# Kernel tuning notes

Measured on AMD Instinct MI355X. Metric: run time of the kernel, lower is better.

Reference implementation:

```python
import jax, jax.numpy as jnp
import numpy as np
from jax import lax

SEQ_LEN = 256
BAT = 128
TAGSET = 64
START_TAG = 62
END_TAG = 63
AVERAGE_BATCH = True


def setup_inputs() -> dict:
    key = jax.random.key(0)
    k1, k2 = jax.random.split(key)
    scores = jax.random.normal(k1, (SEQ_LEN, BAT, TAGSET, TAGSET), dtype=jnp.float32)
    target = jax.random.randint(k2, (SEQ_LEN, BAT, 1), 0, TAGSET * TAGSET, dtype=jnp.int64)
    mask = jnp.ones((SEQ_LEN, BAT), dtype=bool)
    corpus_mask = jnp.ones((1, BAT, 1, TAGSET), dtype=jnp.float32)
    return {"scores": scores, "corpus_mask": corpus_mask, "target": target, "mask": mask}


def _crf_loss(scores, target, mask):
    seq_len, bat, T, _ = scores.shape
    # gold path energy: gather flattened (prev_tag, cur_tag) scores at target indices
    flat = scores.reshape(seq_len, bat, T * T)
    tg = jnp.take_along_axis(flat, target, axis=2)[..., 0]  # [seq_len, bat]
    tg_energy = jnp.sum(jnp.where(mask, tg, 0.0))

    # forward algorithm (log partition) as a scan over time
    init = scores[0, :, START_TAG, :]  # [bat, T]

    def step(carry, inp):
        cur_partition, partition = carry
        cur_values, m = inp  # [bat, T, T], [bat]
        cv = cur_values + cur_partition[:, :, None]          # add prev-tag partition
        new_cur = jax.nn.logsumexp(cv, axis=1)               # [bat, T]
        # switch: where mask is on, take updated partition; else keep old
        new_part = jnp.where(m[:, None], new_cur, partition)
        return (new_cur, new_part), None

    (_, partition), _ = lax.scan(step, (init, init), (scores[1:], mask[1:]))
    log_Z = jnp.sum(partition[:, END_TAG])

    loss = log_Z - tg_energy
    if AVERAGE_BATCH:
        loss = loss / bat
    return loss


def reference(scores, corpus_mask, target, mask):
    # corpus_mask is unused in the unrestricted forward path (as in the original module)
    return _crf_loss(scores, target, mask)
```

## Files before the change

### kernel.cpp

```cpp
#include <hip/hip_runtime.h>

#define NBAT 128
#define NT 64
#define SEQ 256
#define START_TAG 62
#define END_TAG 63

__global__ void zero_out_kernel(float* out) { out[0] = 0.0f; }

__global__ __launch_bounds__(64) void crf_loss_kernel(
    const float* __restrict__ scores,
    const int* __restrict__ target,
    float* __restrict__ out)
{
    const int b    = blockIdx.x;
    const int lane = threadIdx.x;
    const int g    = lane >> 4;
    const int c    = lane & 15;

    __shared__ float cur[NT];

    const size_t matsz   = (size_t)NT * NT;
    const size_t bstride = (size_t)NBAT * matsz;

    float tg = 0.0f;
    for (int t = lane; t < SEQ; t += 64) {
        int idx = target[t * NBAT + b];
        tg += scores[(size_t)t * bstride + (size_t)b * matsz + (size_t)idx];
    }
    #pragma unroll
    for (int off = 1; off < 64; off <<= 1) tg += __shfl_xor(tg, off);

    const float* m0 = scores + (size_t)b * matsz;
    float4 ic = *(const float4*)(m0 + START_TAG * NT + c * 4);
    if (g == 0) *(float4*)(&cur[c * 4]) = ic;
    float C = fmaxf(fmaxf(ic.x, ic.y), fmaxf(ic.z, ic.w));
    #pragma unroll
    for (int off = 1; off < 16; off <<= 1) C = fmaxf(C, __shfl_xor(C, off));

    const int laneoff = g * NT + c * 4;

    float4 v[16], nv[16];
    float4 nc = make_float4(0.f, 0.f, 0.f, 0.f);

    auto step = [&](const float4* vv) {
        float4 s4 = make_float4(0.f, 0.f, 0.f, 0.f);
        #pragma unroll
        for (int r = 0; r < 16; ++r) {
            float cc = cur[g + 4 * r] - C;
            s4.x += __expf(vv[r].x + cc);
            s4.y += __expf(vv[r].y + cc);
            s4.z += __expf(vv[r].z + cc);
            s4.w += __expf(vv[r].w + cc);
        }
        s4.x += __shfl_xor(s4.x, 16); s4.y += __shfl_xor(s4.y, 16);
        s4.z += __shfl_xor(s4.z, 16); s4.w += __shfl_xor(s4.w, 16);
        s4.x += __shfl_xor(s4.x, 32); s4.y += __shfl_xor(s4.y, 32);
        s4.z += __shfl_xor(s4.z, 32); s4.w += __shfl_xor(s4.w, 32);
        nc.x = C + __logf(s4.x);
        nc.y = C + __logf(s4.y);
        nc.z = C + __logf(s4.z);
        nc.w = C + __logf(s4.w);
        if (g == 0) *(float4*)(&cur[c * 4]) = nc;
        float m = fmaxf(fmaxf(nc.x, nc.y), fmaxf(nc.z, nc.w));
        #pragma unroll
        for (int off = 1; off < 16; off <<= 1) m = fmaxf(m, __shfl_xor(m, off));
        C = m;
    };

    {
        const float* p = scores + bstride + (size_t)b * matsz + laneoff;
        #pragma unroll
        for (int r = 0; r < 16; ++r)
            v[r] = *(const float4*)(p + r * 256);
    }

    for (int t = 1; t < SEQ - 1; t += 2) {
        const float* pn = scores + (size_t)(t + 1) * bstride + (size_t)b * matsz + laneoff;
        #pragma unroll
        for (int r = 0; r < 16; ++r)
            nv[r] = *(const float4*)(pn + r * 256);
        step(v);
        const float* pn2 = scores + (size_t)(t + 2) * bstride + (size_t)b * matsz + laneoff;
        #pragma unroll
        for (int r = 0; r < 16; ++r)
            v[r] = *(const float4*)(pn2 + r * 256);
        step(nv);
    }
    step(v);

    float logZb = __shfl(nc.w, 15);
    if (lane == 0) {
        atomicAdd(out, (logZb - tg) * (1.0f / (float)NBAT));
    }
}

extern "C" void kernel_launch(void* const* d_in, const int* in_sizes, int n_in,
                              void* d_out, int out_size, void* d_ws, size_t ws_size,
                              hipStream_t stream) {
    const float* scores = (const float*)d_in[0];
    const int*   target = (const int*)d_in[2];
    float* out = (float*)d_out;

    hipLaunchKernelGGL(zero_out_kernel, dim3(1), dim3(1), 0, stream, out);
    hipLaunchKernelGGL(crf_loss_kernel, dim3(NBAT), dim3(64), 0, stream,
                       scores, target, out);
}
```

Baseline: 817.2 us.

## Parallelize CRF forward over time chunks via bf16 MFMA matrix products in exp space

Replaces the sequential per-batch log-sum-exp scan with a chunked scheme. Each of 16 time chunks per batch item computes a product of exp-space 64x64 transition matrices using bf16 MFMA, with power-of-two rescaling tracked as integer exponents. A second kernel chains the chunk matrices as vector-matrix products and adds the gold-path energy. This exposes 16x more blocks and puts the work on matrix cores, but bf16 exp-space products lose precision. The exponent tracking guards against overflow, but small entries may underflow.

Result: faster. 751.4 us (-8.0%).

```diff
diff --git a/kernel.cpp b/kernel.cpp
--- a/kernel.cpp
+++ b/kernel.cpp
@@ -1,97 +1,212 @@
 #include <hip/hip_runtime.h>
-
+#include <hip/hip_bf16.h>
+
+#define SEQ 256
 #define NBAT 128
 #define NT 64
-#define SEQ 256
 #define START_TAG 62
 #define END_TAG 63
-
-__global__ void zero_out_kernel(float* out) { out[0] = 0.0f; }
-
-__global__ __launch_bounds__(64) void crf_loss_kernel(
+#define CHUNK 16
+#define NCHUNK (SEQ / CHUNK)
+#define TROW 68
+#define LN2 0.6931471805599453f
+
+typedef __bf16 bf16x8 __attribute__((ext_vector_type(8)));
+typedef float f32x4 __attribute__((ext_vector_type(4)));
+
+__global__ __launch_bounds__(64) void crf_chunk_kernel(
+    const float* __restrict__ scores,
+    __hip_bfloat16* __restrict__ wsT,
+    int* __restrict__ wsK,
+    float* __restrict__ out)
+{
+    const int b    = blockIdx.x & (NBAT - 1);
+    const int c    = blockIdx.x >> 7;
+    const int lane = threadIdx.x;
+    const int quad = lane >> 4;
+    const int l15  = lane & 15;
+
+    if (blockIdx.x == 0 && lane == 0) out[0] = 0.0f;
+
+    __shared__ float Pbuf[NT * NT];
+    __shared__ float Tbuf[NT * TROW];
+
+    const int t0 = c * CHUNK;
+    const size_t matfl = (size_t)NT * NT;
+
+    {
+        const float* m1 = scores + ((size_t)((t0 + 1) * NBAT + b)) * matfl;
+        #pragma unroll
+        for (int q = 0; q < 16; ++q) {
+            __builtin_amdgcn_global_load_lds(
+                (const __attribute__((address_space(1))) unsigned int*)(m1 + q * 256 + lane * 4),
+                (__attribute__((address_space(3))) unsigned int*)(&Pbuf[q * 256]),
+                16, 0, 0);
+        }
+    }
+
+    {
+        const float* m0 = scores + ((size_t)(t0 * NBAT + b)) * matfl;
+        #pragma unroll
+        for (int q = 0; q < 16; ++q) {
+            float4 vv = *(const float4*)(m0 + q * 256 + lane * 4);
+            int f = q * 256 + lane * 4;
+            int row = f >> 6, col = f & 63;
+            float4 e;
+            e.x = __expf(vv.x); e.y = __expf(vv.y);
+            e.z = __expf(vv.z); e.w = __expf(vv.w);
+            *(float4*)(&Tbuf[row * TROW + col]) = e;
+        }
+    }
+
+    float r = 1.0f;
+    int ksum = 0;
+    f32x4 acc[4][4];
+
+    for (int s = 1; s < CHUNK; ++s) {
+        asm volatile("s_waitcnt vmcnt(0)" ::: "memory");
+
+        bf16x8 bf[2][4];
+        #pragma unroll
+        for (int ks = 0; ks < 2; ++ks)
+            #pragma unroll
+            for (int nb = 0; nb < 4; ++nb) {
+                const int n  = nb * 16 + l15;
+                const int k0 = ks * 32 + quad * 8;
+                #pragma unroll
+                for (int j = 0; j < 8; ++j)
+                    bf[ks][nb][j] = (__bf16)__expf(Pbuf[(k0 + j) * 64 + n]);
+            }
+
+        asm volatile("s_waitcnt lgkmcnt(0)" ::: "memory");
+        if (s + 1 < CHUNK) {
+            const float* mn = scores + ((size_t)((t0 + s + 1) * NBAT + b)) * matfl;
+            #pragma unroll
+            for (int q = 0; q < 16; ++q) {
+                __builtin_amdgcn_global_load_lds(
+                    (const __attribute__((address_space(1))) unsigned int*)(mn + q * 256 + lane * 4),
+                    (__attribute__((address_space(3))) unsigned int*)(&Pbuf[q * 256]),
+                    16, 0, 0);
+            }
+        }
+
+        bf16x8 af[4][2];
+        #pragma unroll
+        for (int mb = 0; mb < 4; ++mb)
+            #pragma unroll
+            for (int ks = 0; ks < 2; ++ks) {
+                const int m  = mb * 16 + l15;
+                const int k0 = ks * 32 + quad * 8;
+                float4 lo = *(const float4*)(&Tbuf[m * TROW + k0]);
+                float4 hi = *(const float4*)(&Tbuf[m * TROW + k0 + 4]);
+                af[mb][ks][0] = (__bf16)(lo.x * r);
+                af[mb][ks][1] = (__bf16)(lo.y * r);
+                af[mb][ks][2] = (__bf16)(lo.z * r);
+                af[mb][ks][3] = (__bf16)(lo.w * r);
+                af[mb][ks][4] = (__bf16)(hi.x * r);
+                af[mb][ks][5] = (__bf16)(hi.y * r);
+                af[mb][ks][6] = (__bf16)(hi.z * r);
+                af[mb][ks][7] = (__bf16)(hi.w * r);
+            }
+
+        #pragma unroll
+        for (int mb = 0; mb < 4; ++mb)
+            #pragma unroll
+            for (int nb = 0; nb < 4; ++nb) {
+                f32x4 a0 = {0.f, 0.f, 0.f, 0.f};
+                a0 = __builtin_amdgcn_mfma_f32_16x16x32_bf16(af[mb][0], bf[0][nb], a0, 0, 0, 0);
+                a0 = __builtin_amdgcn_mfma_f32_16x16x32_bf16(af[mb][1], bf[1][nb], a0, 0, 0, 0);
+                acc[mb][nb] = a0;
+            }
+
+        if (s < CHUNK - 1) {
+            float mx = 0.0f;
+            #pragma unroll
+            for (int mb = 0; mb < 4; ++mb)
+                #pragma unroll
+                for (int nb = 0; nb < 4; ++nb)
+                    #pragma unroll
+                    for (int reg = 0; reg < 4; ++reg)
+                        mx = fmaxf(mx, acc[mb][nb][reg]);
+            #pragma unroll
+            for (int off = 1; off < 64; off <<= 1)
+                mx = fmaxf(mx, __shfl_xor(mx, off));
+            const int k = (int)((__float_as_uint(mx) >> 23) & 255u) - 127;
+            ksum += k;
+            r = __uint_as_float((unsigned)(127 - k) << 23);
+
+            #pragma unroll
+            for (int mb = 0; mb < 4; ++mb)
+                #pragma unroll
+                for (int nb = 0; nb < 4; ++nb)
+                    #pragma unroll
+                    for (int reg = 0; reg < 4; ++reg) {
+                        const int row = mb * 16 + quad * 4 + reg;
+                        const int col = nb * 16 + l15;
+                        Tbuf[row * TROW + col] = acc[mb][nb][reg];
+                    }
+        }
+    }
+
+    __hip_bfloat16* Tw = wsT + ((size_t)(b * NCHUNK + c)) * matfl;
+    #pragma unroll
+    for (int mb = 0; mb < 4; ++mb)
+        #pragma unroll
+        for (int nb = 0; nb < 4; ++nb)
+            #pragma unroll
+            for (int reg = 0; reg < 4; ++reg) {
+                const int row = mb * 16 + quad * 4 + reg;
+                const int col = nb * 16 + l15;
+                Tw[row * 64 + col] = __float2bfloat16(acc[mb][nb][reg]);
+            }
+    if (lane == 0) wsK[b * NCHUNK + c] = ksum;
+}
+
+__global__ __launch_bounds__(64) void crf_combine_kernel(
     const float* __restrict__ scores,
     const int* __restrict__ target,
+    const __hip_bfloat16* __restrict__ wsT,
+    const int* __restrict__ wsK,
     float* __restrict__ out)
 {
-    const int b    = blockIdx.x;
+    const int b = blockIdx.x;
     const int lane = threadIdx.x;
-    const int g    = lane >> 4;
-    const int c    = lane & 15;
-
-    __shared__ float cur[NT];
-
-    const size_t matsz   = (size_t)NT * NT;
-    const size_t bstride = (size_t)NBAT * matsz;
 
     float tg = 0.0f;
-    for (int t = lane; t < SEQ; t += 64) {
+    #pragma unroll
+    for (int t4 = 0; t4 < 4; ++t4) {
+        int t = t4 * 64 + lane;
         int idx = target[t * NBAT + b];
-        tg += scores[(size_t)t * bstride + (size_t)b * matsz + (size_t)idx];
+        tg += scores[((size_t)(t * NBAT + b)) * 4096 + (size_t)idx];
     }
     #pragma unroll
     for (int off = 1; off < 64; off <<= 1) tg += __shfl_xor(tg, off);
 
-    const float* m0 = scores + (size_t)b * matsz;
-    float4 ic = *(const float4*)(m0 + START_TAG * NT + c * 4);
-    if (g == 0) *(float4*)(&cur[c * 4]) = ic;
-    float C = fmaxf(fmaxf(ic.x, ic.y), fmaxf(ic.z, ic.w));
-    #pragma unroll
-    for (int off = 1; off < 16; off <<= 1) C = fmaxf(C, __shfl_xor(C, off));
-
-    const int laneoff = g * NT + c * 4;
-
-    float4 v[16], nv[16];
-    float4 nc = make_float4(0.f, 0.f, 0.f, 0.f);
-
-    auto step = [&](const float4* vv) {
-        float4 s4 = make_float4(0.f, 0.f, 0.f, 0.f);
-        #pragma unroll
-        for (int r = 0; r < 16; ++r) {
-            float cc = cur[g + 4 * r] - C;
-            s4.x += __expf(vv[r].x + cc);
-            s4.y += __expf(vv[r].y + cc);
-            s4.z += __expf(vv[r].z + cc);
-            s4.w += __expf(vv[r].w + cc);
-        }
-        s4.x += __shfl_xor(s4.x, 16); s4.y += __shfl_xor(s4.y, 16);
-        s4.z += __shfl_xor(s4.z, 16); s4.w += __shfl_xor(s4.w, 16);
-        s4.x += __shfl_xor(s4.x, 32); s4.y += __shfl_xor(s4.y, 32);
-        s4.z += __shfl_xor(s4.z, 32); s4.w += __shfl_xor(s4.w, 32);
-        nc.x = C + __logf(s4.x);
-        nc.y = C + __logf(s4.y);
-        nc.z = C + __logf(s4.z);
-        nc.w = C + __logf(s4.w);
-        if (g == 0) *(float4*)(&cur[c * 4]) = nc;
-        float m = fmaxf(fmaxf(nc.x, nc.y), fmaxf(nc.z, nc.w));
-        #pragma unroll
-        for (int off = 1; off < 16; off <<= 1) m = fmaxf(m, __shfl_xor(m, off));
-        C = m;
-    };
-
-    {
-        const float* p = scores + bstride + (size_t)b * matsz + laneoff;
-        #pragma unroll
-        for (int r = 0; r < 16; ++r)
-            v[r] = *(const float4*)(p + r * 256);
-    }
-
-    for (int t = 1; t < SEQ - 1; t += 2) {
-        const float* pn = scores + (size_t)(t + 1) * bstride + (size_t)b * matsz + laneoff;
-        #pragma unroll
-        for (int r = 0; r < 16; ++r)
-            nv[r] = *(const float4*)(pn + r * 256);
-        step(v);
-        const float* pn2 = scores + (size_t)(t + 2) * bstride + (size_t)b * matsz + laneoff;
-        #pragma unroll
-        for (int r = 0; r < 16; ++r)
-            v[r] = *(const float4*)(pn2 + r * 256);
-        step(nv);
-    }
-    step(v);
-
-    float logZb = __shfl(nc.w, 15);
+    const __hip_bfloat16* T0 = wsT + ((size_t)(b * NCHUNK)) * 4096;
+    float v = __bfloat162float(T0[START_TAG * 64 + lane]);
+    float logacc = (float)wsK[b * NCHUNK] * LN2;
+
+    for (int c = 1; c < NCHUNK; ++c) {
+        const __hip_bfloat16* Tc = wsT + ((size_t)(b * NCHUNK + c)) * 4096;
+        float o = 0.0f;
+        #pragma unroll 8
+        for (int i = 0; i < 64; ++i) {
+            float vi = __shfl(v, i);
+            o += vi * __bfloat162float(Tc[i * 64 + lane]);
+        }
+        float mx = o;
+        #pragma unroll
+        for (int off = 1; off < 64; off <<= 1) mx = fmaxf(mx, __shfl_xor(mx, off));
+        int k = (int)((__float_as_uint(mx) >> 23) & 255u) - 127;
+        o *= __uint_as_float((unsigned)(127 - k) << 23);
+        logacc += (float)(k + wsK[b * NCHUNK + c]) * LN2;
+        v = o;
+    }
+
+    float vend = __shfl(v, END_TAG);
     if (lane == 0) {
-        atomicAdd(out, (logZb - tg) * (1.0f / (float)NBAT));
+        float logZ = logacc + logf(vend);
+        atomicAdd(out, (logZ - tg) * (1.0f / (float)NBAT));
     }
 }
 
@@ -99,10 +214,14 @@
                               void* d_out, int out_size, void* d_ws, size_t ws_size,
                               hipStream_t stream) {
     const float* scores = (const float*)d_in[0];
-    const int*   target = (const int*)d_in[2];
+    const int* target = (const int*)d_in[2];
     float* out = (float*)d_out;
 
-    hipLaunchKernelGGL(zero_out_kernel, dim3(1), dim3(1), 0, stream, out);
-    hipLaunchKernelGGL(crf_loss_kernel, dim3(NBAT), dim3(64), 0, stream,
-                       scores, target, out);
+    __hip_bfloat16* wsT = (__hip_bfloat16*)d_ws;
+    int* wsK = (int*)((char*)d_ws + (size_t)NBAT * NCHUNK * 4096 * 2);
+
+    hipLaunchKernelGGL(crf_chunk_kernel, dim3(NBAT * NCHUNK), dim3(64), 0, stream,
+                       scores, wsT, wsK, out);
+    hipLaunchKernelGGL(crf_combine_kernel, dim3(NBAT), dim3(64), 0, stream,
+                       scores, target, wsT, wsK, out);
 }
```
